# Optimization experiments

Measured on AMD Instinct MI355X. Metric: run time of the kernel, lower is better.

## Reference

```python
import jax, jax.numpy as jnp
import numpy as np

M = 10000      # spans with antecedents
KMAX = 30      # max antecedents per span
N = 12000      # total candidate spans (rows of g_i)
GDIM = 512     # span embedding dim
DDIM, GEDIM, SDIM = 20, 20, 20  # distance / genre / speaker embed dims
HID = 150      # Score hidden dim
GIJ = 3 * GDIM + DDIM + GEDIM + SDIM  # 1596
NDIST, NGENRE, NSPK = 10, 7, 3


def setup_inputs() -> dict:
    rng = np.random.default_rng(0)
    lengths = rng.integers(1, KMAX + 1, size=M)           # antecedents per span
    P = int(lengths.sum())
    seg_ids = np.repeat(np.arange(1, M + 1), lengths).astype(np.int32)  # segment 0 is the leading empty split
    pos_in_seg = np.concatenate([np.arange(l) for l in lengths]).astype(np.int32)
    seg_lengths = np.concatenate([[0], lengths]).astype(np.int32)        # [S], S = M+1
    mention_ids = rng.integers(0, N, size=P).astype(np.int32)
    antecedent_ids = rng.integers(0, N, size=P).astype(np.int32)
    dist_idx = rng.integers(0, NDIST, size=P).astype(np.int32)
    genre_idx = rng.integers(0, NGENRE, size=P).astype(np.int32)
    speaker_idx = rng.integers(0, NSPK, size=P).astype(np.int32)

    ks = jax.random.split(jax.random.key(0), 12)
    sc = lambda d: 1.0 / np.sqrt(d)
    return {
        'g_i': jax.random.normal(ks[0], (N, GDIM), jnp.float32),
        'mention_scores': jax.random.normal(ks[1], (N, 1), jnp.float32),
        'dist_emb': jax.random.normal(ks[2], (NDIST, DDIM), jnp.float32),
        'genre_emb': jax.random.normal(ks[3], (NGENRE, GEDIM), jnp.float32),
        'speaker_emb': jax.random.normal(ks[4], (NSPK, SDIM), jnp.float32),
        'W1': jax.random.normal(ks[5], (GIJ, HID), jnp.float32) * sc(GIJ),
        'b1': jnp.zeros((HID,), jnp.float32),
        'W2': jax.random.normal(ks[6], (HID, HID), jnp.float32) * sc(HID),
        'b2': jnp.zeros((HID,), jnp.float32),
        'W3': jax.random.normal(ks[7], (HID, 1), jnp.float32) * sc(HID),
        'b3': jnp.zeros((1,), jnp.float32),
        'mention_ids': jnp.asarray(mention_ids),
        'antecedent_ids': jnp.asarray(antecedent_ids),
        'dist_idx': jnp.asarray(dist_idx),
        'genre_idx': jnp.asarray(genre_idx),
        'speaker_idx': jnp.asarray(speaker_idx),
        'seg_ids': jnp.asarray(seg_ids),
        'pos_in_seg': jnp.asarray(pos_in_seg),
        'seg_lengths': jnp.asarray(seg_lengths),
    }


def reference(g_i, mention_scores, dist_emb, genre_emb, speaker_emb,
              W1, b1, W2, b2, W3, b3,
              mention_ids, antecedent_ids, dist_idx, genre_idx, speaker_idx,
              seg_ids, pos_in_seg, seg_lengths):
    # phi = cat(distance, genre, speaker) side features, [P, 60]
    phi = jnp.concatenate([dist_emb[dist_idx], genre_emb[genre_idx], speaker_emb[speaker_idx]], axis=1)
    i_g = g_i[mention_ids]      # [P, GDIM] irregular gather
    j_g = g_i[antecedent_ids]   # [P, GDIM]
    pairs = jnp.concatenate([i_g, j_g, i_g * j_g, phi], axis=1)  # [P, GIJ]
    # 3-layer MLP scorer (dropout is identity at inference)
    h = jax.nn.relu(pairs @ W1 + b1)
    h = jax.nn.relu(h @ W2 + b2)
    s_ij = (h @ W3 + b3)[:, 0]  # [P]
    coref = mention_scores[mention_ids, 0] + mention_scores[antecedent_ids, 0] + s_ij  # [P]
    # variable-length segment softmax with epsilon=0 appended, padded with 1000
    S = seg_lengths.shape[0]
    dense = jnp.full((S, KMAX + 1), -jnp.inf, jnp.float32)
    dense = dense.at[seg_ids, pos_in_seg].set(coref)
    dense = dense.at[jnp.arange(S), seg_lengths].set(0.0)  # epsilon slot
    probs = jax.nn.softmax(dense, axis=1)  # -inf slots -> 0
    col = jnp.arange(KMAX + 1)
    probs = jnp.where(col[None, :] > seg_lengths[:, None], 1000.0, probs)  # pad value 1000
    return probs  # [S, KMAX+1]
```

## Files before the change

### kernel.cpp

```cpp
#include <hip/hip_runtime.h>
#include <stdint.h>

#define GDIM   512
#define HID    150
#define HIDP   160
#define NROWS  12000
#define KP1    31
#define BM     128

typedef __attribute__((ext_vector_type(4))) float f32x4;
typedef __attribute__((ext_vector_type(2))) float f32x2;
typedef long i64;

__device__ __forceinline__ unsigned short f2bf(float x){
    unsigned int u = __float_as_uint(x);
    return (unsigned short)((u + 0x7fffu + ((u >> 16) & 1u)) >> 16);
}
__device__ __forceinline__ float bf2f(unsigned short u){
    return __uint_as_float(((unsigned int)u) << 16);
}
__device__ __forceinline__ i64 u2l(uint2 v){ return __builtin_bit_cast(i64, v); }
__device__ __forceinline__ f32x4 mfma8(i64 a, i64 b, f32x4 c){
    return __builtin_amdgcn_mfma_f32_16x16x32_fp8_fp8(a, b, c, 0, 0, 0);
}
__device__ __forceinline__ uint2 f8mulpk(uint2 m, uint2 a){
    f32x2 m0 = __builtin_amdgcn_cvt_pk_f32_fp8(m.x, false);
    f32x2 m1 = __builtin_amdgcn_cvt_pk_f32_fp8(m.x, true);
    f32x2 m2 = __builtin_amdgcn_cvt_pk_f32_fp8(m.y, false);
    f32x2 m3 = __builtin_amdgcn_cvt_pk_f32_fp8(m.y, true);
    f32x2 a0 = __builtin_amdgcn_cvt_pk_f32_fp8(a.x, false);
    f32x2 a1 = __builtin_amdgcn_cvt_pk_f32_fp8(a.x, true);
    f32x2 a2 = __builtin_amdgcn_cvt_pk_f32_fp8(a.y, false);
    f32x2 a3 = __builtin_amdgcn_cvt_pk_f32_fp8(a.y, true);
    unsigned int r0 = 0, r1 = 0;
    r0 = __builtin_amdgcn_cvt_pk_fp8_f32(m0[0]*a0[0], m0[1]*a0[1], r0, false);
    r0 = __builtin_amdgcn_cvt_pk_fp8_f32(m1[0]*a1[0], m1[1]*a1[1], r0, true);
    r1 = __builtin_amdgcn_cvt_pk_fp8_f32(m2[0]*a2[0], m2[1]*a2[1], r1, false);
    r1 = __builtin_amdgcn_cvt_pk_fp8_f32(m3[0]*a3[0], m3[1]*a3[1], r1, true);
    return (uint2){r0, r1};
}
__device__ __forceinline__ void glds16(const void* g, void* l){
    __builtin_amdgcn_global_load_lds(
        (const __attribute__((address_space(1))) unsigned int*)g,
        (__attribute__((address_space(3))) unsigned int*)l, 16, 0, 0);
}

__global__ void k_prep0(const float* __restrict__ g, unsigned char* __restrict__ g8,
                        int* __restrict__ hist, int4* __restrict__ recs,
                        const float* __restrict__ W1, unsigned char* __restrict__ W18,
                        const float* __restrict__ W2, unsigned char* __restrict__ W28, int P){
    int i = blockIdx.x * blockDim.x + threadIdx.x;
    if (i < NROWS) hist[i] = 0;
    if (i < BM) recs[P + i] = (int4){0, 0, (int)0x80000000, 0};
    if (i < 30720){
        int s = i / 10240, r = i % 10240;
        int n = r >> 6, gi = r & 63;
        int gdst = gi ^ (n & 7);
        int k0 = s * 512 + gi * 8;
        float x[8];
        #pragma unroll
        for (int e = 0; e < 8; e++) x[e] = (n < HID) ? W1[(size_t)(k0 + e) * HID + n] : 0.f;
        unsigned int d0 = 0, d1 = 0;
        d0 = __builtin_amdgcn_cvt_pk_fp8_f32(x[0], x[1], d0, false);
        d0 = __builtin_amdgcn_cvt_pk_fp8_f32(x[2], x[3], d0, true);
        d1 = __builtin_amdgcn_cvt_pk_fp8_f32(x[4], x[5], d1, false);
        d1 = __builtin_amdgcn_cvt_pk_fp8_f32(x[6], x[7], d1, true);
        *reinterpret_cast<uint2*>(W18 + (size_t)s * 81920 + n * 512 + gdst * 8) = (uint2){d0, d1};
    }
    if (i < 6912){
        int n2 = i / 42, kd = (i % 42) * 4;
        float y[4];
        #pragma unroll
        for (int e = 0; e < 4; e++){
            int k = kd + e;
            y[e] = (n2 < HID && k < HID) ? W2[(size_t)k * HID + n2] : 0.f;
        }
        unsigned int d = 0;
        d = __builtin_amdgcn_cvt_pk_fp8_f32(y[0], y[1], d, false);
        d = __builtin_amdgcn_cvt_pk_fp8_f32(y[2], y[3], d, true);
        reinterpret_cast<unsigned int*>(W28)[i] = d;
    }
    if (i >= NROWS * 32) return;
    int lh = i & 3, kt = (i >> 2) & 7, row = i >> 5;
    const float* src = g + (size_t)row * 512 + kt * 64 + lh * 8;
    float4 x0 = *reinterpret_cast<const float4*>(src);
    float4 x1 = *reinterpret_cast<const float4*>(src + 4);
    float4 x2 = *reinterpret_cast<const float4*>(src + 32);
    float4 x3 = *reinterpret_cast<const float4*>(src + 36);
    uint4 o; unsigned int d;
    d = 0; d = __builtin_amdgcn_cvt_pk_fp8_f32(x0.x, x0.y, d, false);
    d = __builtin_amdgcn_cvt_pk_fp8_f32(x0.z, x0.w, d, true);  o.x = d;
    d = 0; d = __builtin_amdgcn_cvt_pk_fp8_f32(x1.x, x1.y, d, false);
    d = __builtin_amdgcn_cvt_pk_fp8_f32(x1.z, x1.w, d, true);  o.y = d;
    d = 0; d = __builtin_amdgcn_cvt_pk_fp8_f32(x2.x, x2.y, d, false);
    d = __builtin_amdgcn_cvt_pk_fp8_f32(x2.z, x2.w, d, true);  o.z = d;
    d = 0; d = __builtin_amdgcn_cvt_pk_fp8_f32(x3.x, x3.y, d, false);
    d = __builtin_amdgcn_cvt_pk_fp8_f32(x3.z, x3.w, d, true);  o.w = d;
    *reinterpret_cast<uint4*>(g8 + (size_t)row * 512 + kt * 64 + lh * 16) = o;
}

__global__ void k_wprep(const float* __restrict__ de, const float* __restrict__ ge,
                        const float* __restrict__ se, const float* __restrict__ W1,
                        const float* __restrict__ b1,
                        const float* __restrict__ W3, const float* __restrict__ b2,
                        unsigned short* __restrict__ PhiW,
                        float* __restrict__ w3p, float* __restrict__ b2p){
    int c = blockIdx.x, tid = threadIdx.x;
    if (c < 210 && tid < HIDP){
        int si = c % 3, gi2 = (c / 3) % 7, di = c / 21;
        float acc = 0.f;
        if (tid < HID){
            acc = b1[tid];
            #pragma unroll
            for (int dd = 0; dd < 20; dd++) acc += de[di*20 + dd] * W1[(size_t)(1536 + dd) * HID + tid];
            #pragma unroll
            for (int dd = 0; dd < 20; dd++) acc += ge[gi2*20 + dd] * W1[(size_t)(1556 + dd) * HID + tid];
            #pragma unroll
            for (int dd = 0; dd < 20; dd++) acc += se[si*20 + dd] * W1[(size_t)(1576 + dd) * HID + tid];
        }
        PhiW[c * HIDP + tid] = f2bf(acc);
    }
    if (c == 210 && tid < HIDP){
        w3p[tid] = (tid < HID) ? W3[tid] : 0.f;
        b2p[tid] = (tid < HID) ? b2[tid] : 0.f;
    }
}

__global__ void k_hist(const int* __restrict__ mid, int* __restrict__ hist, int P){
    int p = blockIdx.x * blockDim.x + threadIdx.x;
    if (p < P) atomicAdd(&hist[mid[p]], 1);
}
__global__ void k_scan(const int* __restrict__ hist, int* __restrict__ offsw, int nb){
    __shared__ int part[1024];
    int t = threadIdx.x;
    int chunk = (nb + 1023) / 1024;
    int lo = t * chunk, hi = lo + chunk; if (hi > nb) hi = nb;
    int s = 0;
    for (int b = lo; b < hi; b++) s += hist[b];
    part[t] = s;
    __syncthreads();
    for (int d = 1; d < 1024; d <<= 1){
        int v = (t >= d) ? part[t - d] : 0;
        __syncthreads();
        part[t] += v;
        __syncthreads();
    }
    int run = part[t] - s;
    for (int b = lo; b < hi; b++){ offsw[b] = run; run += hist[b]; }
}
__global__ void k_scatter(const int* __restrict__ mident, const int* __restrict__ antid,
                          const int* __restrict__ di, const int* __restrict__ gi, const int* __restrict__ si,
                          const int* __restrict__ seg, const int* __restrict__ pos, const float* __restrict__ ms,
                          int* __restrict__ offsw, int4* __restrict__ recs, int P){
    int p = blockIdx.x * blockDim.x + threadIdx.x;
    if (p >= P) return;
    int m = mident[p], a = antid[p];
    int idx = atomicAdd(&offsw[m], 1);
    int combo = (di[p] * 7 + gi[p]) * 3 + si[p];
    int meta = (combo << 19) | (seg[p] << 5) | pos[p];
    int4 r; r.x = m; r.y = a; r.z = meta; r.w = __float_as_int(ms[m] + ms[a]);
    recs[idx] = r;
}

__global__ __launch_bounds__(256) void k_proj(const unsigned char* __restrict__ g8,
                                              const unsigned char* __restrict__ W18,
                                              unsigned char* __restrict__ out){
    __shared__ __align__(16) char smem[81920];
    const unsigned char* Wt = W18 + (size_t)blockIdx.y * 81920;
    unsigned char* outh = out + (size_t)blockIdx.y * NROWS * HIDP;
    int tid = threadIdx.x, lane = tid & 63, w = tid >> 6;
    int l15 = lane & 15, lh = lane >> 4;
    int swz8 = (l15 & 7) << 3;
    int row0 = blockIdx.x * BM;

    int r0 = row0 + 32*w + l15;       int r0c = (r0 < NROWS) ? r0 : NROWS - 1;
    int r1 = r0 + 16;                 int r1c = (r1 < NROWS) ? r1 : NROWS - 1;
    const unsigned char* gp0 = g8 + (size_t)r0c * GDIM + lh * 16;
    const unsigned char* gp1 = g8 + (size_t)r1c * GDIM + lh * 16;

    #pragma unroll
    for (int i = 0; i < 20; i++){
        int c = w * 20 + i;
        glds16(Wt + c * 1024 + lane * 16, smem + c * 1024);
    }

    f32x4 acc1[10][2];
    #pragma unroll
    for (int t = 0; t < 10; t++){ acc1[t][0] = (f32x4){0,0,0,0}; acc1[t][1] = (f32x4){0,0,0,0}; }

    asm volatile("s_waitcnt vmcnt(0)" ::: "memory");
    __builtin_amdgcn_s_barrier();

    uint4 R0 = *reinterpret_cast<const uint4*>(gp0);
    uint4 R1 = *reinterpret_cast<const uint4*>(gp1);
    #pragma unroll
    for (int kt = 0; kt < 8; kt++){
        uint4 N0, N1;
        if (kt < 7){
            N0 = *reinterpret_cast<const uint4*>(gp0 + (kt+1)*64);
            N1 = *reinterpret_cast<const uint4*>(gp1 + (kt+1)*64);
        }
        i64 a00 = u2l((uint2){R0.x, R0.y}), a01 = u2l((uint2){R0.z, R0.w});
        i64 a10 = u2l((uint2){R1.x, R1.y}), a11 = u2l((uint2){R1.z, R1.w});
        #pragma unroll
        for (int t = 0; t < 10; t++){
            int rowb = (t*16 + l15) * 512;
            i64 b0 = *reinterpret_cast<const i64*>(&smem[rowb + ((kt*64 +  0 + lh*8) ^ swz8)]);
            i64 b1 = *reinterpret_cast<const i64*>(&smem[rowb + ((kt*64 + 32 + lh*8) ^ swz8)]);
            acc1[t][0] = mfma8(b0, a00, acc1[t][0]);
            acc1[t][1] = mfma8(b0, a10, acc1[t][1]);
            acc1[t][0] = mfma8(b1, a01, acc1[t][0]);
            acc1[t][1] = mfma8(b1, a11, acc1[t][1]);
        }
        R0 = N0; R1 = N1;
    }

    #pragma unroll
    for (int rf = 0; rf < 2; rf++){
        int row = row0 + 32*w + 16*rf + l15;
        if (row < NROWS){
            #pragma unroll
            for (int t = 0; t < 10; t++){
                f32x4 a = acc1[t][rf];
                unsigned int dw = 0;
                dw = __builtin_amdgcn_cvt_pk_fp8_f32(a[0], a[1], dw, false);
                dw = __builtin_amdgcn_cvt_pk_fp8_f32(a[2], a[3], dw, true);
                *reinterpret_cast<unsigned int*>(outh + (size_t)row * HIDP + 16*t + 4*lh) = dw;
            }
        }
    }
}

__global__ __launch_bounds__(256) void k_fused(
    const unsigned char* __restrict__ g8,
    const unsigned char* __restrict__ W1c8, const unsigned char* __restrict__ W28,
    const unsigned short* __restrict__ PhiW, const unsigned char* __restrict__ Am,
    const unsigned char* __restrict__ Aa,
    const float* __restrict__ w3p, const float* __restrict__ b2p, const float* __restrict__ b3,
    const int4* __restrict__ recs,
    float* __restrict__ dense)
{
    __shared__ __align__(16) char smem[81920];
    int tid = threadIdx.x, lane = tid & 63, w = tid >> 6;
    int l15 = lane & 15, lh = lane >> 4;
    int swz8 = (l15 & 7) << 3;
    int p0 = blockIdx.x * BM;

    int4 rec0 = recs[p0 + 32*w + l15];
    int4 rec1 = recs[p0 + 32*w + 16 + l15];

    const unsigned char* gm0 = g8 + (size_t)rec0.x * GDIM + lh * 16;
    const unsigned char* ga0 = g8 + (size_t)rec0.y * GDIM + lh * 16;
    const unsigned char* gm1 = g8 + (size_t)rec1.x * GDIM + lh * 16;
    const unsigned char* ga1 = g8 + (size_t)rec1.y * GDIM + lh * 16;

    #pragma unroll
    for (int i = 0; i < 20; i++){
        int c = w * 20 + i;
        glds16(W1c8 + c * 1024 + lane * 16, smem + c * 1024);
    }

    f32x4 acc1[10][2];
    #pragma unroll
    for (int t = 0; t < 10; t++){ acc1[t][0] = (f32x4){0,0,0,0}; acc1[t][1] = (f32x4){0,0,0,0}; }

    asm volatile("s_waitcnt vmcnt(0)" ::: "memory");
    __builtin_amdgcn_s_barrier();

    uint4 Rm0 = *reinterpret_cast<const uint4*>(gm0);
    uint4 Ra0 = *reinterpret_cast<const uint4*>(ga0);
    uint4 Rm1 = *reinterpret_cast<const uint4*>(gm1);
    uint4 Ra1 = *reinterpret_cast<const uint4*>(ga1);
    #pragma unroll
    for (int kt = 0; kt < 8; kt++){
        uint4 Nm0, Na0, Nm1, Na1;
        if (kt < 7){
            Nm0 = *reinterpret_cast<const uint4*>(gm0 + (kt+1)*64);
            Na0 = *reinterpret_cast<const uint4*>(ga0 + (kt+1)*64);
            Nm1 = *reinterpret_cast<const uint4*>(gm1 + (kt+1)*64);
            Na1 = *reinterpret_cast<const uint4*>(ga1 + (kt+1)*64);
        }
        uint2 p00 = f8mulpk((uint2){Rm0.x, Rm0.y}, (uint2){Ra0.x, Ra0.y});
        uint2 p01 = f8mulpk((uint2){Rm0.z, Rm0.w}, (uint2){Ra0.z, Ra0.w});
        uint2 p10 = f8mulpk((uint2){Rm1.x, Rm1.y}, (uint2){Ra1.x, Ra1.y});
        uint2 p11 = f8mulpk((uint2){Rm1.z, Rm1.w}, (uint2){Ra1.z, Ra1.w});
        i64 lp00 = u2l(p00), lp01 = u2l(p01), lp10 = u2l(p10), lp11 = u2l(p11);
        #pragma unroll
        for (int t = 0; t < 10; t++){
            int rowb = (t*16 + l15) * 512;
            i64 b0 = *reinterpret_cast<const i64*>(&smem[rowb + ((kt*64 +  0 + lh*8) ^ swz8)]);
            i64 b1 = *reinterpret_cast<const i64*>(&smem[rowb + ((kt*64 + 32 + lh*8) ^ swz8)]);
            acc1[t][0] = mfma8(b0, lp00, acc1[t][0]);
            acc1[t][1] = mfma8(b0, lp10, acc1[t][1]);
            acc1[t][0] = mfma8(b1, lp01, acc1[t][0]);
            acc1[t][1] = mfma8(b1, lp11, acc1[t][1]);
        }
        Rm0 = Nm0; Ra0 = Na0; Rm1 = Nm1; Ra1 = Na1;
    }

    asm volatile("s_waitcnt lgkmcnt(0)" ::: "memory");
    __builtin_amdgcn_s_barrier();

    #pragma unroll
    for (int i = 0; i < 7; i++){
        int c = w * 7 + i;
        if (c < 27) glds16(W28 + c * 1024 + lane * 16, smem + 21504 + c * 1024);
    }

    #pragma unroll
    for (int rf = 0; rf < 2; rf++){
        int4 rc = rf ? rec1 : rec0;
        int pr = 32*w + 16*rf + l15;
        const unsigned char* amp = Am + (size_t)rc.x * HIDP;
        const unsigned char* aap = Aa + (size_t)rc.y * HIDP;
        int combo = (rc.z >> 19) & 0xFF;
        const unsigned short* php = PhiW + (size_t)combo * HIDP;
        char* h1row = smem + pr * 168;
        #pragma unroll
        for (int t = 0; t < 10; t++){
            int h0 = 16*t + 4*lh;
            unsigned int amd = *reinterpret_cast<const unsigned int*>(amp + h0);
            unsigned int aad = *reinterpret_cast<const unsigned int*>(aap + h0);
            ushort4 ph4 = *reinterpret_cast<const ushort4*>(php + h0);
            f32x2 amL = __builtin_amdgcn_cvt_pk_f32_fp8(amd, false);
            f32x2 amH = __builtin_amdgcn_cvt_pk_f32_fp8(amd, true);
            f32x2 aaL = __builtin_amdgcn_cvt_pk_f32_fp8(aad, false);
            f32x2 aaH = __builtin_amdgcn_cvt_pk_f32_fp8(aad, true);
            f32x4 a = acc1[t][rf];
            float v0 = fmaxf(a[0] + amL[0] + aaL[0] + bf2f(ph4.x), 0.f);
            float v1 = fmaxf(a[1] + amL[1] + aaL[1] + bf2f(ph4.y), 0.f);
            float v2 = fmaxf(a[2] + amH[0] + aaH[0] + bf2f(ph4.z), 0.f);
            float v3 = fmaxf(a[3] + amH[1] + aaH[1] + bf2f(ph4.w), 0.f);
            unsigned int dw = 0;
            dw = __builtin_amdgcn_cvt_pk_fp8_f32(v0, v1, dw, false);
            dw = __builtin_amdgcn_cvt_pk_fp8_f32(v2, v3, dw, true);
            *reinterpret_cast<unsigned int*>(h1row + h0) = dw;
        }
    }

    asm volatile("s_waitcnt vmcnt(0) lgkmcnt(0)" ::: "memory");
    __builtin_amdgcn_s_barrier();

    f32x4 acc2[10][2];
    #pragma unroll
    for (int t = 0; t < 10; t++){ acc2[t][0] = (f32x4){0,0,0,0}; acc2[t][1] = (f32x4){0,0,0,0}; }
    const char* w2b = smem + 21504;
    #pragma unroll
    for (int k2 = 0; k2 < 5; k2++){
        i64 h0f = *reinterpret_cast<const i64*>(smem + (32*w + l15)      * 168 + k2*32 + lh*8);
        i64 h1f = *reinterpret_cast<const i64*>(smem + (32*w + 16 + l15) * 168 + k2*32 + lh*8);
        #pragma unroll
        for (int t = 0; t < 10; t++){
            i64 wf = *reinterpret_cast<const i64*>(w2b + (16*t + l15) * 168 + k2*32 + lh*8);
            acc2[t][0] = mfma8(wf, h0f, acc2[t][0]);
            acc2[t][1] = mfma8(wf, h1f, acc2[t][1]);
        }
    }

    float b3v = b3[0];
    #pragma unroll
    for (int rf = 0; rf < 2; rf++){
        int4 rc = rf ? rec1 : rec0;
        float s = 0.f;
        #pragma unroll
        for (int t = 0; t < 10; t++){
            f32x4 w3v = *reinterpret_cast<const f32x4*>(w3p + 16*t + 4*lh);
            f32x4 b2v = *reinterpret_cast<const f32x4*>(b2p + 16*t + 4*lh);
            f32x4 a = acc2[t][rf];
            s += fmaxf(a[0] + b2v[0], 0.f) * w3v[0];
            s += fmaxf(a[1] + b2v[1], 0.f) * w3v[1];
            s += fmaxf(a[2] + b2v[2], 0.f) * w3v[2];
            s += fmaxf(a[3] + b2v[3], 0.f) * w3v[3];
        }
        s += __shfl_xor(s, 16);
        s += __shfl_xor(s, 32);
        if (!(rc.z & 0x80000000) && lh == 0){
            float val = s + b3v + __int_as_float(rc.w);
            dense[(size_t)((rc.z >> 5) & 0x3FFF) * KP1 + (rc.z & 31)] = val;
        }
    }
}

__global__ void k_softmax(const float* __restrict__ dense, const int* __restrict__ seg_lengths,
                          float* __restrict__ out, int S){
    int wid = threadIdx.x >> 6, lane = threadIdx.x & 63;
    int s = blockIdx.x * 4 + wid;
    if (s >= S) return;
    int len = seg_lengths[s];
    float ninf = -__builtin_inff();
    float val = ninf;
    if (lane < KP1) val = (lane < len) ? dense[(size_t)s * KP1 + lane] : ((lane == len) ? 0.f : ninf);
    float m = val;
    #pragma unroll
    for (int msk = 1; msk < 64; msk <<= 1) m = fmaxf(m, __shfl_xor(m, msk));
    float e = expf(val - m);
    float sum = e;
    #pragma unroll
    for (int msk = 1; msk < 64; msk <<= 1) sum += __shfl_xor(sum, msk);
    if (lane < KP1) out[(size_t)s * KP1 + lane] = (lane > len) ? 1000.f : (e / sum);
}

extern "C" void kernel_launch(void* const* d_in, const int* in_sizes, int n_in,
                              void* d_out, int out_size, void* d_ws, size_t ws_size,
                              hipStream_t stream){
    const float* g_i        = (const float*)d_in[0];
    const float* ms         = (const float*)d_in[1];
    const float* dist_emb   = (const float*)d_in[2];
    const float* genre_emb  = (const float*)d_in[3];
    const float* spk_emb    = (const float*)d_in[4];
    const float* W1         = (const float*)d_in[5];
    const float* b1         = (const float*)d_in[6];
    const float* W2         = (const float*)d_in[7];
    const float* b2         = (const float*)d_in[8];
    const float* W3         = (const float*)d_in[9];
    const float* b3         = (const float*)d_in[10];
    const int* mention_ids  = (const int*)d_in[11];
    const int* antecedent_ids = (const int*)d_in[12];
    const int* dist_idx     = (const int*)d_in[13];
    const int* genre_idx    = (const int*)d_in[14];
    const int* spk_idx      = (const int*)d_in[15];
    const int* seg_ids      = (const int*)d_in[16];
    const int* pos_in_seg   = (const int*)d_in[17];
    const int* seg_lengths  = (const int*)d_in[18];
    int P = in_sizes[11];
    int S = in_sizes[18];

    char* ws = (char*)d_ws;
    unsigned char* W18   = (unsigned char*)(ws + 0);
    unsigned char* W28   = (unsigned char*)(ws + 245760);
    unsigned short* PhiW = (unsigned short*)(ws + 273408);
    float* w3pad         = (float*)(ws + 340608);
    float* b2pad         = (float*)(ws + 341248);
    unsigned char* g8    = (unsigned char*)(ws + 341888);
    unsigned char* Am8   = (unsigned char*)(ws + 6485888);
    unsigned char* Aa8   = (unsigned char*)(ws + 8405888);
    int* hist            = (int*)(ws + 10325888);
    int* offsw           = (int*)(ws + 10373888);
    int4* recs           = (int4*)(ws + 10421888);
    float* dense         = (float*)(ws + 13000192);

    k_prep0<<<1500, 256, 0, stream>>>(g_i, g8, hist, recs, W1, W18, W2, W28, P);
    k_wprep<<<211, 256, 0, stream>>>(dist_emb, genre_emb, spk_emb, W1, b1, W3, b2,
                                     PhiW, w3pad, b2pad);
    k_hist<<<(P + 255)/256, 256, 0, stream>>>(mention_ids, hist, P);
    k_scan<<<1, 1024, 0, stream>>>(hist, offsw, NROWS);
    k_scatter<<<(P + 255)/256, 256, 0, stream>>>(mention_ids, antecedent_ids, dist_idx, genre_idx,
        spk_idx, seg_ids, pos_in_seg, ms, offsw, recs, P);

    k_proj<<<dim3((NROWS + BM - 1)/BM, 2), 256, 0, stream>>>(g8, W18, Am8);

    k_fused<<<(P + BM - 1)/BM, 256, 0, stream>>>(g8, W18 + 2*81920, W28, PhiW,
        Am8, Aa8, w3pad, b2pad, b3, recs, dense);

    k_softmax<<<(S + 3)/4, 256, 0, stream>>>(dense, seg_lengths, (float*)d_out, S);
}
```

Before: 116.3 us.

## Deepen global-load prefetch in GEMM loops, remap fused blocks per XCD, merge prep kernels

The A-operand loads in k_proj and k_fused now use a three-deep register ring that prefetches two k-steps ahead, and the first barrier waits only for the LDS weight copy rather than all outstanding global loads. k_fused remaps block indices so that each XCD processes a contiguous range of record tiles, which should improve L2 locality for the sorted mention gathers. The separate k_wprep launch is folded into k_prep0 as extra thread ranges, removing one kernel launch. The cost is higher register pressure from the extra in-flight buffers, which may reduce occupancy.

```diff
diff --git a/kernel.cpp b/kernel.cpp
--- a/kernel.cpp
+++ b/kernel.cpp
@@ -6,7 +6,8 @@
 #define HIDP   160
 #define NROWS  12000
 #define KP1    31
-#define BM     128
+#define BMP    128
+#define BMF    128
 
 typedef __attribute__((ext_vector_type(4))) float f32x4;
 typedef __attribute__((ext_vector_type(2))) float f32x2;
@@ -48,10 +49,15 @@
 __global__ void k_prep0(const float* __restrict__ g, unsigned char* __restrict__ g8,
                         int* __restrict__ hist, int4* __restrict__ recs,
                         const float* __restrict__ W1, unsigned char* __restrict__ W18,
-                        const float* __restrict__ W2, unsigned char* __restrict__ W28, int P){
+                        const float* __restrict__ W2, unsigned char* __restrict__ W28,
+                        const float* __restrict__ de, const float* __restrict__ ge,
+                        const float* __restrict__ se, const float* __restrict__ b1,
+                        const float* __restrict__ W3, const float* __restrict__ b2,
+                        unsigned short* __restrict__ PhiW,
+                        float* __restrict__ w3p, float* __restrict__ b2p, int P){
     int i = blockIdx.x * blockDim.x + threadIdx.x;
     if (i < NROWS) hist[i] = 0;
-    if (i < BM) recs[P + i] = (int4){0, 0, (int)0x80000000, 0};
+    if (i < BMF) recs[P + i] = (int4){0, 0, (int)0x80000000, 0};
     if (i < 30720){
         int s = i / 10240, r = i % 10240;
         int n = r >> 6, gi = r & 63;
@@ -80,49 +86,42 @@
         d = __builtin_amdgcn_cvt_pk_fp8_f32(y[2], y[3], d, true);
         reinterpret_cast<unsigned int*>(W28)[i] = d;
     }
-    if (i >= NROWS * 32) return;
-    int lh = i & 3, kt = (i >> 2) & 7, row = i >> 5;
-    const float* src = g + (size_t)row * 512 + kt * 64 + lh * 8;
-    float4 x0 = *reinterpret_cast<const float4*>(src);
-    float4 x1 = *reinterpret_cast<const float4*>(src + 4);
-    float4 x2 = *reinterpret_cast<const float4*>(src + 32);
-    float4 x3 = *reinterpret_cast<const float4*>(src + 36);
-    uint4 o; unsigned int d;
-    d = 0; d = __builtin_amdgcn_cvt_pk_fp8_f32(x0.x, x0.y, d, false);
-    d = __builtin_amdgcn_cvt_pk_fp8_f32(x0.z, x0.w, d, true);  o.x = d;
-    d = 0; d = __builtin_amdgcn_cvt_pk_fp8_f32(x1.x, x1.y, d, false);
-    d = __builtin_amdgcn_cvt_pk_fp8_f32(x1.z, x1.w, d, true);  o.y = d;
-    d = 0; d = __builtin_amdgcn_cvt_pk_fp8_f32(x2.x, x2.y, d, false);
-    d = __builtin_amdgcn_cvt_pk_fp8_f32(x2.z, x2.w, d, true);  o.z = d;
-    d = 0; d = __builtin_amdgcn_cvt_pk_fp8_f32(x3.x, x3.y, d, false);
-    d = __builtin_amdgcn_cvt_pk_fp8_f32(x3.z, x3.w, d, true);  o.w = d;
-    *reinterpret_cast<uint4*>(g8 + (size_t)row * 512 + kt * 64 + lh * 16) = o;
-}
-
-__global__ void k_wprep(const float* __restrict__ de, const float* __restrict__ ge,
-                        const float* __restrict__ se, const float* __restrict__ W1,
-                        const float* __restrict__ b1,
-                        const float* __restrict__ W3, const float* __restrict__ b2,
-                        unsigned short* __restrict__ PhiW,
-                        float* __restrict__ w3p, float* __restrict__ b2p){
-    int c = blockIdx.x, tid = threadIdx.x;
-    if (c < 210 && tid < HIDP){
+    if (i < NROWS * 32){
+        int lh = i & 3, kt = (i >> 2) & 7, row = i >> 5;
+        const float* src = g + (size_t)row * 512 + kt * 64 + lh * 8;
+        float4 x0 = *reinterpret_cast<const float4*>(src);
+        float4 x1 = *reinterpret_cast<const float4*>(src + 4);
+        float4 x2 = *reinterpret_cast<const float4*>(src + 32);
+        float4 x3 = *reinterpret_cast<const float4*>(src + 36);
+        uint4 o; unsigned int d;
+        d = 0; d = __builtin_amdgcn_cvt_pk_fp8_f32(x0.x, x0.y, d, false);
+        d = __builtin_amdgcn_cvt_pk_fp8_f32(x0.z, x0.w, d, true);  o.x = d;
+        d = 0; d = __builtin_amdgcn_cvt_pk_fp8_f32(x1.x, x1.y, d, false);
+        d = __builtin_amdgcn_cvt_pk_fp8_f32(x1.z, x1.w, d, true);  o.y = d;
+        d = 0; d = __builtin_amdgcn_cvt_pk_fp8_f32(x2.x, x2.y, d, false);
+        d = __builtin_amdgcn_cvt_pk_fp8_f32(x2.z, x2.w, d, true);  o.z = d;
+        d = 0; d = __builtin_amdgcn_cvt_pk_fp8_f32(x3.x, x3.y, d, false);
+        d = __builtin_amdgcn_cvt_pk_fp8_f32(x3.z, x3.w, d, true);  o.w = d;
+        *reinterpret_cast<uint4*>(g8 + (size_t)row * 512 + kt * 64 + lh * 16) = o;
+    } else if (i < NROWS * 32 + 33600){
+        int j = i - NROWS * 32;
+        int c = j / HIDP, h = j - c * HIDP;
         int si = c % 3, gi2 = (c / 3) % 7, di = c / 21;
         float acc = 0.f;
-        if (tid < HID){
-            acc = b1[tid];
+        if (h < HID){
+            acc = b1[h];
             #pragma unroll
-            for (int dd = 0; dd < 20; dd++) acc += de[di*20 + dd] * W1[(size_t)(1536 + dd) * HID + tid];
+            for (int dd = 0; dd < 20; dd++) acc += de[di*20 + dd] * W1[(size_t)(1536 + dd) * HID + h];
             #pragma unroll
-            for (int dd = 0; dd < 20; dd++) acc += ge[gi2*20 + dd] * W1[(size_t)(1556 + dd) * HID + tid];
+            for (int dd = 0; dd < 20; dd++) acc += ge[gi2*20 + dd] * W1[(size_t)(1556 + dd) * HID + h];
             #pragma unroll
-            for (int dd = 0; dd < 20; dd++) acc += se[si*20 + dd] * W1[(size_t)(1576 + dd) * HID + tid];
-        }
-        PhiW[c * HIDP + tid] = f2bf(acc);
-    }
-    if (c == 210 && tid < HIDP){
-        w3p[tid] = (tid < HID) ? W3[tid] : 0.f;
-        b2p[tid] = (tid < HID) ? b2[tid] : 0.f;
+            for (int dd = 0; dd < 20; dd++) acc += se[si*20 + dd] * W1[(size_t)(1576 + dd) * HID + h];
+        }
+        PhiW[c * HIDP + h] = f2bf(acc);
+    } else if (i < NROWS * 32 + 33600 + HIDP){
+        int h = i - NROWS * 32 - 33600;
+        w3p[h] = (h < HID) ? W3[h] : 0.f;
+        b2p[h] = (h < HID) ? b2[h] : 0.f;
     }
 }
 
@@ -171,7 +170,7 @@
     int tid = threadIdx.x, lane = tid & 63, w = tid >> 6;
     int l15 = lane & 15, lh = lane >> 4;
     int swz8 = (l15 & 7) << 3;
-    int row0 = blockIdx.x * BM;
+    int row0 = blockIdx.x * BMP;
 
     int r0 = row0 + 32*w + l15;       int r0c = (r0 < NROWS) ? r0 : NROWS - 1;
     int r1 = r0 + 16;                 int r1c = (r1 < NROWS) ? r1 : NROWS - 1;
@@ -188,32 +187,40 @@
     #pragma unroll
     for (int t = 0; t < 10; t++){ acc1[t][0] = (f32x4){0,0,0,0}; acc1[t][1] = (f32x4){0,0,0,0}; }
 
-    asm volatile("s_waitcnt vmcnt(0)" ::: "memory");
+#define LOADAP(kt, R) do{ \
+    R[0] = *reinterpret_cast<const uint4*>(gp0 + (kt)*64); \
+    R[1] = *reinterpret_cast<const uint4*>(gp1 + (kt)*64); \
+}while(0)
+#define COMPP(kt, R) do{ \
+    i64 a00 = u2l((uint2){R[0].x, R[0].y}), a01 = u2l((uint2){R[0].z, R[0].w}); \
+    i64 a10 = u2l((uint2){R[1].x, R[1].y}), a11 = u2l((uint2){R[1].z, R[1].w}); \
+    _Pragma("unroll") \
+    for (int t = 0; t < 10; t++){ \
+        int rowb = (t*16 + l15) * 512; \
+        i64 b0 = *reinterpret_cast<const i64*>(&smem[rowb + (((kt)*64 +  0 + lh*8) ^ swz8)]); \
+        i64 b1 = *reinterpret_cast<const i64*>(&smem[rowb + (((kt)*64 + 32 + lh*8) ^ swz8)]); \
+        acc1[t][0] = mfma8(b0, a00, acc1[t][0]); \
+        acc1[t][1] = mfma8(b0, a10, acc1[t][1]); \
+        acc1[t][0] = mfma8(b1, a01, acc1[t][0]); \
+        acc1[t][1] = mfma8(b1, a11, acc1[t][1]); \
+    } \
+}while(0)
+
+    uint4 A0[2], A1[2], A2[2];
+    LOADAP(0, A0); LOADAP(1, A1);
+    asm volatile("s_waitcnt vmcnt(4)" ::: "memory");
     __builtin_amdgcn_s_barrier();
 
-    uint4 R0 = *reinterpret_cast<const uint4*>(gp0);
-    uint4 R1 = *reinterpret_cast<const uint4*>(gp1);
-    #pragma unroll
-    for (int kt = 0; kt < 8; kt++){
-        uint4 N0, N1;
-        if (kt < 7){
-            N0 = *reinterpret_cast<const uint4*>(gp0 + (kt+1)*64);
-            N1 = *reinterpret_cast<const uint4*>(gp1 + (kt+1)*64);
-        }
-        i64 a00 = u2l((uint2){R0.x, R0.y}), a01 = u2l((uint2){R0.z, R0.w});
-        i64 a10 = u2l((uint2){R1.x, R1.y}), a11 = u2l((uint2){R1.z, R1.w});
-        #pragma unroll
-        for (int t = 0; t < 10; t++){
-            int rowb = (t*16 + l15) * 512;
-            i64 b0 = *reinterpret_cast<const i64*>(&smem[rowb + ((kt*64 +  0 + lh*8) ^ swz8)]);
-            i64 b1 = *reinterpret_cast<const i64*>(&smem[rowb + ((kt*64 + 32 + lh*8) ^ swz8)]);
-            acc1[t][0] = mfma8(b0, a00, acc1[t][0]);
-            acc1[t][1] = mfma8(b0, a10, acc1[t][1]);
-            acc1[t][0] = mfma8(b1, a01, acc1[t][0]);
-            acc1[t][1] = mfma8(b1, a11, acc1[t][1]);
-        }
-        R0 = N0; R1 = N1;
-    }
+    LOADAP(2, A2); COMPP(0, A0);
+    LOADAP(3, A0); COMPP(1, A1);
+    LOADAP(4, A1); COMPP(2, A2);
+    LOADAP(5, A2); COMPP(3, A0);
+    LOADAP(6, A0); COMPP(4, A1);
+    LOADAP(7, A1); COMPP(5, A2);
+    COMPP(6, A0);
+    COMPP(7, A1);
+#undef LOADAP
+#undef COMPP
 
     #pragma unroll
     for (int rf = 0; rf < 2; rf++){
@@ -244,7 +251,14 @@
     int tid = threadIdx.x, lane = tid & 63, w = tid >> 6;
     int l15 = lane & 15, lh = lane >> 4;
     int swz8 = (l15 & 7) << 3;
-    int p0 = blockIdx.x * BM;
+
+    int nwg = gridDim.x, orig = blockIdx.x, bid = orig;
+    if (nwg >= 8){
+        int q = nwg >> 3, r = nwg & 7;
+        int xcd = orig & 7, lid = orig >> 3;
+        bid = (xcd < r ? xcd * (q + 1) : r * (q + 1) + (xcd - r) * q) + lid;
+    }
+    int p0 = bid * BMF;
 
     int4 rec0 = recs[p0 + 32*w + l15];
     int4 rec1 = recs[p0 + 32*w + 16 + l15];
@@ -264,39 +278,45 @@
     #pragma unroll
     for (int t = 0; t < 10; t++){ acc1[t][0] = (f32x4){0,0,0,0}; acc1[t][1] = (f32x4){0,0,0,0}; }
 
-    asm volatile("s_waitcnt vmcnt(0)" ::: "memory");
+#define LOADAF(kt, R) do{ \
+    R[0] = *reinterpret_cast<const uint4*>(gm0 + (kt)*64); \
+    R[1] = *reinterpret_cast<const uint4*>(ga0 + (kt)*64); \
+    R[2] = *reinterpret_cast<const uint4*>(gm1 + (kt)*64); \
+    R[3] = *reinterpret_cast<const uint4*>(ga1 + (kt)*64); \
+}while(0)
+#define COMPF(kt, R) do{ \
+    uint2 p00 = f8mulpk((uint2){R[0].x, R[0].y}, (uint2){R[1].x, R[1].y}); \
+    uint2 p01 = f8mulpk((uint2){R[0].z, R[0].w}, (uint2){R[1].z, R[1].w}); \
+    uint2 p10 = f8mulpk((uint2){R[2].x, R[2].y}, (uint2){R[3].x, R[3].y}); \
+    uint2 p11 = f8mulpk((uint2){R[2].z, R[2].w}, (uint2){R[3].z, R[3].w}); \
+    i64 lp00 = u2l(p00), lp01 = u2l(p01), lp10 = u2l(p10), lp11 = u2l(p11); \
+    _Pragma("unroll") \
+    for (int t = 0; t < 10; t++){ \
+        int rowb = (t*16 + l15) * 512; \
+        i64 b0 = *reinterpret_cast<const i64*>(&smem[rowb + (((kt)*64 +  0 + lh*8) ^ swz8)]); \
+        i64 b1 = *reinterpret_cast<const i64*>(&smem[rowb + (((kt)*64 + 32 + lh*8) ^ swz8)]); \
+        acc1[t][0] = mfma8(b0, lp00, acc1[t][0]); \
+        acc1[t][1] = mfma8(b0, lp10, acc1[t][1]); \
+        acc1[t][0] = mfma8(b1, lp01, acc1[t][0]); \
+        acc1[t][1] = mfma8(b1, lp11, acc1[t][1]); \
+    } \
+}while(0)
+
+    uint4 A0[4], A1[4], A2[4];
+    LOADAF(0, A0); LOADAF(1, A1);
+    asm volatile("s_waitcnt vmcnt(8)" ::: "memory");
     __builtin_amdgcn_s_barrier();
 
-    uint4 Rm0 = *reinterpret_cast<const uint4*>(gm0);
-    uint4 Ra0 = *reinterpret_cast<const uint4*>(ga0);
-    uint4 Rm1 = *reinterpret_cast<const uint4*>(gm1);
-    uint4 Ra1 = *reinterpret_cast<const uint4*>(ga1);
-    #pragma unroll
-    for (int kt = 0; kt < 8; kt++){
-        uint4 Nm0, Na0, Nm1, Na1;
-        if (kt < 7){
-            Nm0 = *reinterpret_cast<const uint4*>(gm0 + (kt+1)*64);
-            Na0 = *reinterpret_cast<const uint4*>(ga0 + (kt+1)*64);
-            Nm1 = *reinterpret_cast<const uint4*>(gm1 + (kt+1)*64);
-            Na1 = *reinterpret_cast<const uint4*>(ga1 + (kt+1)*64);
-        }
-        uint2 p00 = f8mulpk((uint2){Rm0.x, Rm0.y}, (uint2){Ra0.x, Ra0.y});
-        uint2 p01 = f8mulpk((uint2){Rm0.z, Rm0.w}, (uint2){Ra0.z, Ra0.w});
-        uint2 p10 = f8mulpk((uint2){Rm1.x, Rm1.y}, (uint2){Ra1.x, Ra1.y});
-        uint2 p11 = f8mulpk((uint2){Rm1.z, Rm1.w}, (uint2){Ra1.z, Ra1.w});
-        i64 lp00 = u2l(p00), lp01 = u2l(p01), lp10 = u2l(p10), lp11 = u2l(p11);
-        #pragma unroll
-        for (int t = 0; t < 10; t++){
-            int rowb = (t*16 + l15) * 512;
-            i64 b0 = *reinterpret_cast<const i64*>(&smem[rowb + ((kt*64 +  0 + lh*8) ^ swz8)]);
-            i64 b1 = *reinterpret_cast<const i64*>(&smem[rowb + ((kt*64 + 32 + lh*8) ^ swz8)]);
-            acc1[t][0] = mfma8(b0, lp00, acc1[t][0]);
-            acc1[t][1] = mfma8(b0, lp10, acc1[t][1]);
-            acc1[t][0] = mfma8(b1, lp01, acc1[t][0]);
-            acc1[t][1] = mfma8(b1, lp11, acc1[t][1]);
-        }
-        Rm0 = Nm0; Ra0 = Na0; Rm1 = Nm1; Ra1 = Na1;
-    }
+    LOADAF(2, A2); COMPF(0, A0);
+    LOADAF(3, A0); COMPF(1, A1);
+    LOADAF(4, A1); COMPF(2, A2);
+    LOADAF(5, A2); COMPF(3, A0);
+    LOADAF(6, A0); COMPF(4, A1);
+    LOADAF(7, A1); COMPF(5, A2);
+    COMPF(6, A0);
+    COMPF(7, A1);
+#undef LOADAF
+#undef COMPF
 
     asm volatile("s_waitcnt lgkmcnt(0)" ::: "memory");
     __builtin_amdgcn_s_barrier();
@@ -439,17 +459,17 @@
     int4* recs           = (int4*)(ws + 10421888);
     float* dense         = (float*)(ws + 13000192);
 
-    k_prep0<<<1500, 256, 0, stream>>>(g_i, g8, hist, recs, W1, W18, W2, W28, P);
-    k_wprep<<<211, 256, 0, stream>>>(dist_emb, genre_emb, spk_emb, W1, b1, W3, b2,
-                                     PhiW, w3pad, b2pad);
+    int prep_threads = NROWS * 32 + 33600 + HIDP;
+    k_prep0<<<(prep_threads + 255)/256, 256, 0, stream>>>(g_i, g8, hist, recs, W1, W18, W2, W28,
+        dist_emb, genre_emb, spk_emb, b1, W3, b2, PhiW, w3pad, b2pad, P);
     k_hist<<<(P + 255)/256, 256, 0, stream>>>(mention_ids, hist, P);
     k_scan<<<1, 1024, 0, stream>>>(hist, offsw, NROWS);
     k_scatter<<<(P + 255)/256, 256, 0, stream>>>(mention_ids, antecedent_ids, dist_idx, genre_idx,
         spk_idx, seg_ids, pos_in_seg, ms, offsw, recs, P);
 
-    k_proj<<<dim3((NROWS + BM - 1)/BM, 2), 256, 0, stream>>>(g8, W18, Am8);
-
-    k_fused<<<(P + BM - 1)/BM, 256, 0, stream>>>(g8, W18 + 2*81920, W28, PhiW,
+    k_proj<<<dim3((NROWS + BMP - 1)/BMP, 2), 256, 0, stream>>>(g8, W18, Am8);
+
+    k_fused<<<(P + BMF - 1)/BMF, 256, 0, stream>>>(g8, W18 + 2*81920, W28, PhiW,
         Am8, Aa8, w3pad, b2pad, b3, recs, dense);
 
     k_softmax<<<(S + 3)/4, 256, 0, stream>>>(dense, seg_lengths, (float*)d_out, S);
```

After: 115.2 us. Within noise of the previous version (-0.9%).
